# Kernel tuning notes

Hardware: AMD Instinct MI355X
Metric: run time of the kernel (lower is better)

Reference implementation:

```python
import jax, jax.numpy as jnp
import numpy as np

BRANCH = 4
DEPTH = 8  # complete 4-ary tree, levels 0..8 (leaves are level 0)
X_SIZE = 512
H_SIZE = 512


def _build_tree():
    N = sum(BRANCH ** d for d in range(DEPTH + 1))  # 87381
    depth = np.zeros(N, dtype=np.int32)
    start = 1
    for d in range(1, DEPTH + 1):
        c = BRANCH ** d
        depth[start:start + c] = d
        start += c
    node_level = (DEPTH - depth).astype(np.int32)  # topological height, leaves=0
    src = np.arange(1, N, dtype=np.int32)          # child
    dst = (src - 1) // BRANCH                      # parent
    return N, src, dst.astype(np.int32), node_level


def setup_inputs() -> dict:
    key = jax.random.key(0)
    k = jax.random.split(key, 6)
    N, src, dst, node_level = _build_tree()
    sx = 1.0 / np.sqrt(X_SIZE)
    sh = 1.0 / np.sqrt(H_SIZE)
    return {
        "x": jax.random.normal(k[0], (N, X_SIZE), jnp.float32),
        "W_w": jax.random.normal(k[1], (3 * H_SIZE, X_SIZE), jnp.float32) * sx,
        "b_w": jax.random.normal(k[2], (3 * H_SIZE,), jnp.float32) * sx,
        "U_r": jax.random.normal(k[3], (H_SIZE, H_SIZE), jnp.float32) * sh,
        "U_hc": jax.random.normal(k[4], (H_SIZE, H_SIZE), jnp.float32) * sh,
        "U_z": jax.random.normal(k[5], (H_SIZE, H_SIZE), jnp.float32) * sh,
        "edge_src": jnp.asarray(src),
        "edge_dst": jnp.asarray(dst),
        "node_level": jnp.asarray(node_level),
        "num_levels": DEPTH + 1,
    }


def reference(x, W_w, b_w, U_r, U_hc, U_z, edge_src, edge_dst, node_level, num_levels):
    hs = U_r.shape[0]
    n = x.shape[0]
    wx = x @ W_w.T + b_w                      # (n, 3h)
    wrx = wx[:, :hs]
    whx = wx[:, hs:2 * hs]
    wzx = wx[:, 2 * hs:]
    edge_level = node_level[edge_dst]         # level of parent receiving the message

    # Leaves: mailbox is a single zero 'z' slot -> z = sigmoid(w_z_x), h_pre = 0
    h_leaf = (1.0 - jax.nn.sigmoid(wzx)) * jnp.tanh(whx)
    h = jnp.where((node_level == 0)[:, None], h_leaf, 0.0)

    for l in range(1, num_levels):
        emask = (edge_level == l).astype(x.dtype)[:, None]   # (E,1)
        hsrc = h[edge_src] * emask                            # masked child states (E,h)
        h_sum = jax.ops.segment_sum(hsrc, edge_dst, num_segments=n)  # sum of children
        r = jax.nn.sigmoid(wrx + h_sum @ U_r.T)
        h_cand = jnp.tanh(whx + (r * h_sum) @ U_hc.T)
        z_e = hsrc @ U_z.T                                    # raw U_z(h_child), (E,h)
        # reduce: h_pre = sum_children z_raw * h_child (no sigmoid, faithful to source)
        h_pre = jax.ops.segment_sum(z_e * hsrc, edge_dst, num_segments=n)
        # update: z = sigmoid(z_raw + w_z_x), summed over children
        z_sig_sum = jax.ops.segment_sum(
            jax.nn.sigmoid(z_e + wzx[edge_dst]) * emask, edge_dst, num_segments=n)
        h_new = h_pre + (1.0 - z_sig_sum) * h_cand
        h = jnp.where((node_level == l)[:, None], h_new, h)
    return h
```

## Files before the change

### kernel.cpp

```cpp
#include <hip/hip_runtime.h>


#define NNODES 87381
#define NINT   21845
#define NLEAF  65536

typedef __attribute__((ext_vector_type(8))) __bf16 bf16x8;
typedef __attribute__((ext_vector_type(4))) float f32x4;

__device__ __forceinline__ float sigmoidf_(float x) { return 1.0f / (1.0f + __expf(-x)); }
__device__ __forceinline__ float tanhf_(float x) { return 2.0f / (1.0f + __expf(-2.0f * x)) - 1.0f; }

__device__ __forceinline__ unsigned short bf_rne(float f) {
  unsigned int u = __float_as_uint(f);
  unsigned int r = u + 0x7FFFu + ((u >> 16) & 1u);
  return (unsigned short)(r >> 16);
}
__device__ __forceinline__ void split2(float f, unsigned short& h, unsigned short& l) {
  h = bf_rne(f);
  l = bf_rne(f - __uint_as_float((unsigned int)h << 16));
}
__device__ __forceinline__ float bf2f(unsigned short h) {
  return __uint_as_float((unsigned int)h << 16);
}

__device__ __forceinline__ int xcd_remap(int h, int nwg) {
  const int q = nwg >> 3, r = nwg & 7;
  const int xcd = h & 7, slot = h >> 3;
  return (xcd < r ? xcd * (q + 1) : r * (q + 1) + (xcd - r) * q) + slot;
}

__global__ __launch_bounds__(256) void split_k(const float* __restrict__ s,
                                               unsigned short* __restrict__ hi,
                                               unsigned short* __restrict__ lo, int n4) {
  int i = blockIdx.x * 256 + threadIdx.x;
  if (i >= n4) return;
  float4 v = *(const float4*)(s + (size_t)i * 4);
  ushort4 h, l;
  split2(v.x, h.x, l.x); split2(v.y, h.y, l.y);
  split2(v.z, h.z, l.z); split2(v.w, h.w, l.w);
  *(ushort4*)(hi + (size_t)i * 4) = h;
  *(ushort4*)(lo + (size_t)i * 4) = l;
}

template <bool CLAMP>
__device__ __forceinline__ void stage_half(const unsigned short* __restrict__ g,
                                           int rows_left, unsigned short* l0,
                                           int lane, int c0) {
#pragma unroll
  for (int c = c0; c < c0 + 4; ++c) {
    const int lr = c * 16 + (lane >> 2);
    const int gr = CLAMP ? (lr < rows_left ? lr : rows_left - 1) : lr;
    const int sg = (lane & 3) ^ ((lr >> 1) & 3);
    __builtin_amdgcn_global_load_lds(
        (const __attribute__((address_space(1))) void*)(g + (size_t)gr * 512 + sg * 8),
        (__attribute__((address_space(3))) void*)(l0 + c * 512), 16, 0, 0);
  }
}

template <int EPI>
__global__ __launch_bounds__(512, 4) void mgemm(const unsigned short* __restrict__ Ah,
                                                const unsigned short* __restrict__ Al,
                                                const unsigned short* __restrict__ Bh,
                                                const unsigned short* __restrict__ Bl,
                                                float* __restrict__ C, int ldc, int M,
                                                const float* __restrict__ wx, int g0,
                                                const float* __restrict__ bias,
                                                const unsigned short* __restrict__ FH,
                                                const unsigned short* __restrict__ FL,
                                                unsigned short* __restrict__ Oh,
                                                unsigned short* __restrict__ Ol,
                                                int nnb) {
  __shared__ unsigned short As_h[2][128][32];
  __shared__ unsigned short As_l[2][128][32];
  __shared__ unsigned short Bs_h[2][128][32];
  __shared__ unsigned short Bs_l[2][128][32];
  const int t = threadIdx.x;
  const int lane = t & 63, wave = t >> 6;
  const int wm = wave & 1, wn = wave >> 1;
  const int L = xcd_remap(blockIdx.x, gridDim.x);
  const int m0 = (L / nnb) * 128, n0 = (L % nnb) * 128;

  f32x4 acc[4][2];
#pragma unroll
  for (int i = 0; i < 4; ++i)
#pragma unroll
    for (int j = 0; j < 2; ++j) acc[i][j] = (f32x4){0.f, 0.f, 0.f, 0.f};

  const int fr = lane & 15, fg = lane >> 4;

  auto stage = [&](int buf, int k0) {
    const int c0 = (wave & 1) * 4;
    switch (wave >> 1) {
      case 0: stage_half<true >(Ah + (size_t)m0 * 512 + k0, M - m0, &As_h[buf][0][0], lane, c0); break;
      case 1: stage_half<true >(Al + (size_t)m0 * 512 + k0, M - m0, &As_l[buf][0][0], lane, c0); break;
      case 2: stage_half<false>(Bh + (size_t)n0 * 512 + k0, 0, &Bs_h[buf][0][0], lane, c0); break;
      default: stage_half<false>(Bl + (size_t)n0 * 512 + k0, 0, &Bs_l[buf][0][0], lane, c0); break;
    }
  };

  auto comp = [&](int buf) {
    bf16x8 ah[4], al[4], bh[2], bl[2];
#pragma unroll
    for (int mt = 0; mt < 4; ++mt) {
      const int row = wm * 64 + mt * 16 + fr;
      const int gp = (fg ^ ((row >> 1) & 3)) * 8;
      ah[mt] = *(const bf16x8*)&As_h[buf][row][gp];
      al[mt] = *(const bf16x8*)&As_l[buf][row][gp];
    }
#pragma unroll
    for (int nt = 0; nt < 2; ++nt) {
      const int row = wn * 32 + nt * 16 + fr;
      const int gp = (fg ^ ((row >> 1) & 3)) * 8;
      bh[nt] = *(const bf16x8*)&Bs_h[buf][row][gp];
      bl[nt] = *(const bf16x8*)&Bs_l[buf][row][gp];
    }
#pragma unroll
    for (int mt = 0; mt < 4; ++mt)
#pragma unroll
      for (int nt = 0; nt < 2; ++nt) {
        acc[mt][nt] = __builtin_amdgcn_mfma_f32_16x16x32_bf16(ah[mt], bh[nt], acc[mt][nt], 0, 0, 0);
        acc[mt][nt] = __builtin_amdgcn_mfma_f32_16x16x32_bf16(ah[mt], bl[nt], acc[mt][nt], 0, 0, 0);
        acc[mt][nt] = __builtin_amdgcn_mfma_f32_16x16x32_bf16(al[mt], bh[nt], acc[mt][nt], 0, 0, 0);
      }
  };

  stage(0, 0);
  __syncthreads();
  for (int kk = 0; kk < 16; kk += 2) {
    stage(1, (kk + 1) * 32);
    comp(0);
    __syncthreads();
    if (kk < 14) stage(0, (kk + 2) * 32);
    comp(1);
    __syncthreads();
  }

  const int ecol = lane & 15;
  const int erow = (lane >> 4) * 4;

  if (EPI == 4) {
#pragma unroll
    for (int mt = 0; mt < 4; ++mt) {
#pragma unroll
      for (int nt = 0; nt < 2; ++nt) {
        const int col = n0 + wn * 32 + nt * 16 + ecol;
        const int row0 = m0 + wm * 64 + mt * 16 + erow;
        if (row0 >= M) continue;
        const int p = row0 >> 2;
        const float wz = wx[(size_t)(g0 + p) * 1536 + 1024 + col];
        float hpre = 0.f, zs = 0.f;
#pragma unroll
        for (int r = 0; r < 4; ++r) {
          const float zev = acc[mt][nt][r];
          const float hch = bias[(size_t)(row0 + r) * 512 + col];
          hpre = fmaf(zev, hch, hpre);
          zs += sigmoidf_(zev + wz);
        }
        float* po = C + (size_t)p * 512 + col;
        const float hc = *po;
        const float res = hpre + (1.f - zs) * hc;
        *po = res;
        unsigned short oh, ol;
        split2(res, oh, ol);
        Oh[(size_t)p * 512 + col] = oh;
        Ol[(size_t)p * 512 + col] = ol;
      }
    }
    return;
  }

#pragma unroll
  for (int mt = 0; mt < 4; ++mt) {
#pragma unroll
    for (int nt = 0; nt < 2; ++nt) {
      const int col = n0 + wn * 32 + nt * 16 + ecol;
#pragma unroll
      for (int r = 0; r < 4; ++r) {
        const int row = m0 + wm * 64 + mt * 16 + erow + r;
        if (row >= M) continue;
        const float v = acc[mt][nt][r];
        if (EPI == 1) {
          const size_t ix = (size_t)row * 512 + col;
          const float hs = bf2f(FH[ix]) + bf2f(FL[ix]);
          const float rg = sigmoidf_(wx[(size_t)(g0 + row) * 1536 + col] + v);
          unsigned short oh, ol;
          split2(rg * hs, oh, ol);
          Oh[ix] = oh;
          Ol[ix] = ol;
        } else if (EPI == 2) {
          C[(size_t)row * ldc + col] = tanhf_(wx[(size_t)(g0 + row) * 1536 + 512 + col] + v);
        } else {
          C[(size_t)row * ldc + col] = v + bias[col];
        }
      }
    }
  }
}

__global__ __launch_bounds__(512, 4) void mleaf(const unsigned short* __restrict__ xh,
                                                const unsigned short* __restrict__ xl,
                                                const unsigned short* __restrict__ Wh,
                                                const unsigned short* __restrict__ Wl,
                                                const float* __restrict__ bw,
                                                float* __restrict__ out,
                                                unsigned short* __restrict__ hcH,
                                                unsigned short* __restrict__ hcL) {
  __shared__ unsigned short As_h[2][128][32];
  __shared__ unsigned short As_l[2][128][32];
  __shared__ unsigned short Bs_h[2][128][32];
  __shared__ unsigned short Bs_l[2][128][32];
  const int t = threadIdx.x;
  const int lane = t & 63, wave = t >> 6;
  const int wm = wave & 1, wn = wave >> 1;
  const int L = xcd_remap(blockIdx.x, gridDim.x);
  const int m0 = (L >> 3) * 128, n0 = (L & 7) * 64;

  f32x4 acch[4], accz[4];
#pragma unroll
  for (int i = 0; i < 4; ++i) {
    acch[i] = (f32x4){0.f, 0.f, 0.f, 0.f};
    accz[i] = (f32x4){0.f, 0.f, 0.f, 0.f};
  }

  const int fr = lane & 15, fg = lane >> 4;

  auto stage = [&](int buf, int k0) {
    const int c0 = (wave & 1) * 4;
    const int grp = wave >> 1;
    if (grp == 0) {
      stage_half<false>(xh + (size_t)m0 * 512 + k0, 0, &As_h[buf][0][0], lane, c0);
    } else if (grp == 1) {
      stage_half<false>(xl + (size_t)m0 * 512 + k0, 0, &As_l[buf][0][0], lane, c0);
    } else {
      const unsigned short* Ws = (grp == 2) ? Wh : Wl;
      unsigned short* dst = (grp == 2) ? &Bs_h[buf][0][0] : &Bs_l[buf][0][0];
#pragma unroll
      for (int c = c0; c < c0 + 4; ++c) {
        const int lr = c * 16 + (lane >> 2);
        const int grow = (lr < 64) ? (512 + n0 + lr) : (1024 + n0 + (lr - 64));
        const int sg = (lane & 3) ^ ((lr >> 1) & 3);
        __builtin_amdgcn_global_load_lds(
            (const __attribute__((address_space(1))) void*)(Ws + (size_t)grow * 512 + k0 + sg * 8),
            (__attribute__((address_space(3))) void*)(dst + c * 512), 16, 0, 0);
      }
    }
  };

  auto comp = [&](int buf) {
    bf16x8 ah[4], al[4], bhh, bhl, bzh, bzl;
    {
      const int rh_ = wn * 16 + fr;
      const int rz_ = 64 + rh_;
      const int gph = (fg ^ ((rh_ >> 1) & 3)) * 8;
      const int gpz = (fg ^ ((rz_ >> 1) & 3)) * 8;
      bhh = *(const bf16x8*)&Bs_h[buf][rh_][gph];
      bhl = *(const bf16x8*)&Bs_l[buf][rh_][gph];
      bzh = *(const bf16x8*)&Bs_h[buf][rz_][gpz];
      bzl = *(const bf16x8*)&Bs_l[buf][rz_][gpz];
    }
#pragma unroll
    for (int mt = 0; mt < 4; ++mt) {
      const int row = wm * 64 + mt * 16 + fr;
      const int gp = (fg ^ ((row >> 1) & 3)) * 8;
      ah[mt] = *(const bf16x8*)&As_h[buf][row][gp];
      al[mt] = *(const bf16x8*)&As_l[buf][row][gp];
    }
#pragma unroll
    for (int mt = 0; mt < 4; ++mt) {
      acch[mt] = __builtin_amdgcn_mfma_f32_16x16x32_bf16(ah[mt], bhh, acch[mt], 0, 0, 0);
      acch[mt] = __builtin_amdgcn_mfma_f32_16x16x32_bf16(ah[mt], bhl, acch[mt], 0, 0, 0);
      acch[mt] = __builtin_amdgcn_mfma_f32_16x16x32_bf16(al[mt], bhh, acch[mt], 0, 0, 0);
      accz[mt] = __builtin_amdgcn_mfma_f32_16x16x32_bf16(ah[mt], bzh, accz[mt], 0, 0, 0);
      accz[mt] = __builtin_amdgcn_mfma_f32_16x16x32_bf16(ah[mt], bzl, accz[mt], 0, 0, 0);
      accz[mt] = __builtin_amdgcn_mfma_f32_16x16x32_bf16(al[mt], bzh, accz[mt], 0, 0, 0);
    }
  };

  stage(0, 0);
  __syncthreads();
  for (int kk = 0; kk < 16; kk += 2) {
    stage(1, (kk + 1) * 32);
    comp(0);
    __syncthreads();
    if (kk < 14) stage(0, (kk + 2) * 32);
    comp(1);
    __syncthreads();
  }

  const int ecol = lane & 15;
  const int erow = (lane >> 4) * 4;
  const int col = n0 + wn * 16 + ecol;
  const float bh_ = bw[512 + col];
  const float bz_ = bw[1024 + col];
#pragma unroll
  for (int mt = 0; mt < 4; ++mt) {
#pragma unroll
    for (int r = 0; r < 4; ++r) {
      const int row = m0 + wm * 64 + mt * 16 + erow + r;
      const float vh = acch[mt][r] + bh_;
      const float vz = accz[mt][r] + bz_;
      const float hval = (1.f - sigmoidf_(vz)) * tanhf_(vh);
      out[(size_t)(NINT + row) * 512 + col] = hval;
      unsigned short oh, ol;
      split2(hval, oh, ol);
      const size_t ix = (size_t)row * 512 + col;
      hcH[ix] = oh;
      hcL[ix] = ol;
    }
  }
}

__global__ __launch_bounds__(256) void child_sum_k(const float* __restrict__ out,
                                                   int cbase, int nl,
                                                   unsigned short* __restrict__ hH,
                                                   unsigned short* __restrict__ hL) {
  const int idx = blockIdx.x * 256 + threadIdx.x;
  if (idx >= nl * 128) return;
  const int i = idx >> 7;
  const int jq = (idx & 127) << 2;
  const float* b = out + (size_t)(cbase + 4 * i) * 512 + jq;
  const float4 a = *(const float4*)(b);
  const float4 c = *(const float4*)(b + 512);
  const float4 d = *(const float4*)(b + 1024);
  const float4 e = *(const float4*)(b + 1536);
  float4 s;
  s.x = a.x + c.x + d.x + e.x;
  s.y = a.y + c.y + d.y + e.y;
  s.z = a.z + c.z + d.z + e.z;
  s.w = a.w + c.w + d.w + e.w;
  ushort4 sh, sl;
  split2(s.x, sh.x, sl.x); split2(s.y, sh.y, sl.y);
  split2(s.z, sh.z, sl.z); split2(s.w, sh.w, sl.w);
  *(ushort4*)(hH + (size_t)i * 512 + jq) = sh;
  *(ushort4*)(hL + (size_t)i * 512 + jq) = sl;
}

extern "C" void kernel_launch(void* const* d_in, const int* in_sizes, int n_in,
                              void* d_out, int out_size, void* d_ws, size_t ws_size,
                              hipStream_t stream) {
  const float* x   = (const float*)d_in[0];
  const float* Ww  = (const float*)d_in[1];
  const float* bw  = (const float*)d_in[2];
  const float* Ur  = (const float*)d_in[3];
  const float* Uhc = (const float*)d_in[4];
  const float* Uz  = (const float*)d_in[5];
  float* out = (float*)d_out;

  char* p = (char*)d_ws;
  unsigned short* x_hi = (unsigned short*)p;
  unsigned short* x_lo = x_hi + (size_t)NNODES * 512;
  unsigned short* rhH = (unsigned short*)p;
  unsigned short* rhL = rhH + (size_t)16384 * 512;
  p += (size_t)NNODES * 512 * 4;
  float* wx_int = (float*)p;                 p += (size_t)NINT * 1536 * 4;
  unsigned short* hsH = (unsigned short*)p;  p += (size_t)16384 * 512 * 2;
  unsigned short* hsL = (unsigned short*)p;  p += (size_t)16384 * 512 * 2;
  unsigned short* hcH = (unsigned short*)p;  p += (size_t)65536 * 512 * 2;
  unsigned short* hcL = (unsigned short*)p;  p += (size_t)65536 * 512 * 2;
  unsigned short* hc2H = (unsigned short*)p; p += (size_t)16384 * 512 * 2;
  unsigned short* hc2L = (unsigned short*)p; p += (size_t)16384 * 512 * 2;
  unsigned short* W_hi = (unsigned short*)p;   p += (size_t)1536 * 512 * 2;
  unsigned short* W_lo = (unsigned short*)p;   p += (size_t)1536 * 512 * 2;
  unsigned short* Ur_hi = (unsigned short*)p;  p += (size_t)512 * 512 * 2;
  unsigned short* Ur_lo = (unsigned short*)p;  p += (size_t)512 * 512 * 2;
  unsigned short* Uhc_hi = (unsigned short*)p; p += (size_t)512 * 512 * 2;
  unsigned short* Uhc_lo = (unsigned short*)p; p += (size_t)512 * 512 * 2;
  unsigned short* Uz_hi = (unsigned short*)p;  p += (size_t)512 * 512 * 2;
  unsigned short* Uz_lo = (unsigned short*)p;  p += (size_t)512 * 512 * 2;

  split_k<<<(1536 * 512 / 4 + 255) / 256, 256, 0, stream>>>(Ww, W_hi, W_lo, 1536 * 512 / 4);
  split_k<<<(512 * 512 / 4 + 255) / 256, 256, 0, stream>>>(Ur, Ur_hi, Ur_lo, 512 * 512 / 4);
  split_k<<<(512 * 512 / 4 + 255) / 256, 256, 0, stream>>>(Uhc, Uhc_hi, Uhc_lo, 512 * 512 / 4);
  split_k<<<(512 * 512 / 4 + 255) / 256, 256, 0, stream>>>(Uz, Uz_hi, Uz_lo, 512 * 512 / 4);
  split_k<<<((int)((size_t)NNODES * 512 / 4) + 255) / 256, 256, 0, stream>>>(
      x, x_hi, x_lo, (int)((size_t)NNODES * 512 / 4));

  mgemm<3><<<((NINT + 127) / 128) * 12, 512, 0, stream>>>(
      x_hi, x_lo, W_hi, W_lo, wx_int, 1536, NINT, nullptr, 0, bw,
      nullptr, nullptr, nullptr, nullptr, 12);

  mleaf<<<(NLEAF / 128) * 8, 512, 0, stream>>>(
      x_hi + (size_t)NINT * 512, x_lo + (size_t)NINT * 512, W_hi, W_lo, bw, out, hcH, hcL);

  static const int S[10] = {0, 1, 5, 21, 85, 341, 1365, 5461, 21845, 87381};
  unsigned short *rdH = hcH, *rdL = hcL, *wrH = hc2H, *wrL = hc2L;
  for (int l = 1; l <= 8; ++l) {
    const int d = 8 - l;
    const int pbase = S[d];
    const int nl = S[d + 1] - S[d];
    const int cbase = S[d + 1];
    const int el = 4 * nl;

    child_sum_k<<<(nl * 128 + 255) / 256, 256, 0, stream>>>(out, cbase, nl, hsH, hsL);

    const int grm = (nl + 127) / 128;
    mgemm<1><<<grm * 4, 512, 0, stream>>>(hsH, hsL, Ur_hi, Ur_lo, nullptr, 512, nl,
                                          wx_int, pbase, nullptr, hsH, hsL, rhH, rhL, 4);
    mgemm<2><<<grm * 4, 512, 0, stream>>>(rhH, rhL, Uhc_hi, Uhc_lo,
                                          out + (size_t)pbase * 512, 512, nl,
                                          wx_int, pbase, nullptr, nullptr, nullptr,
                                          nullptr, nullptr, 4);
    const int gzm = (el + 127) / 128;
    mgemm<4><<<gzm * 4, 512, 0, stream>>>(rdH, rdL, Uz_hi, Uz_lo,
                                          out + (size_t)pbase * 512, 512, el,
                                          wx_int, pbase, out + (size_t)cbase * 512,
                                          nullptr, nullptr, wrH, wrL, 4);
    unsigned short* tH = rdH; rdH = wrH; wrH = tH;
    unsigned short* tL = rdL; rdL = wrL; wrL = tL;
  }
}
```

Before: 1.420 ms.

## Fuse the last four small tree levels into one single-block persistent kernel

Levels 5 through 8 of the tree have only 64, 16, 4 and 1 parent nodes. These were previously handled by 16 separate kernel launches, each mostly idle. A single 1024-thread block now runs the child sum, the three GEMMs and their epilogues for these levels, with block-wide barriers between stages. This removes launch and tail latency, at the cost of running the small GEMMs on one compute unit, where each wave must stream the full weight matrices from memory.

```diff
diff --git a/kernel.cpp b/kernel.cpp
--- a/kernel.cpp
+++ b/kernel.cpp
@@ -336,6 +336,153 @@
   *(ushort4*)(hL + (size_t)i * 512 + jq) = sl;
 }
 
+__device__ __forceinline__ void tail_gemm(
+    int M, const unsigned short* __restrict__ AH, const unsigned short* __restrict__ AL,
+    const unsigned short* __restrict__ BH, const unsigned short* __restrict__ BL,
+    int wave, int lane, int epi, const float* __restrict__ wx, int g0,
+    float* __restrict__ C, const unsigned short* __restrict__ FH,
+    const unsigned short* __restrict__ FL, unsigned short* __restrict__ OH,
+    unsigned short* __restrict__ OL, const float* __restrict__ childh) {
+  const int fr = lane & 15, fq = (lane >> 4) * 8;
+  const int n0 = wave * 32;
+  const int ecol = lane & 15, erow = (lane >> 4) * 4;
+  for (int mc = 0; mc < M; mc += 64) {
+    f32x4 acc[4][2];
+#pragma unroll
+    for (int i = 0; i < 4; ++i) {
+      acc[i][0] = (f32x4){0.f, 0.f, 0.f, 0.f};
+      acc[i][1] = (f32x4){0.f, 0.f, 0.f, 0.f};
+    }
+#pragma unroll 2
+    for (int k0 = 0; k0 < 512; k0 += 32) {
+      bf16x8 ah[4], al[4], bh[2], bl[2];
+#pragma unroll
+      for (int nt = 0; nt < 2; ++nt) {
+        const size_t bo = (size_t)(n0 + nt * 16 + fr) * 512 + k0 + fq;
+        bh[nt] = *(const bf16x8*)(BH + bo);
+        bl[nt] = *(const bf16x8*)(BL + bo);
+      }
+#pragma unroll
+      for (int mt = 0; mt < 4; ++mt) {
+        int row = mc + mt * 16 + fr;
+        if (row >= M) row = M - 1;
+        const size_t ao = (size_t)row * 512 + k0 + fq;
+        ah[mt] = *(const bf16x8*)(AH + ao);
+        al[mt] = *(const bf16x8*)(AL + ao);
+      }
+#pragma unroll
+      for (int mt = 0; mt < 4; ++mt)
+#pragma unroll
+        for (int nt = 0; nt < 2; ++nt) {
+          acc[mt][nt] = __builtin_amdgcn_mfma_f32_16x16x32_bf16(ah[mt], bh[nt], acc[mt][nt], 0, 0, 0);
+          acc[mt][nt] = __builtin_amdgcn_mfma_f32_16x16x32_bf16(ah[mt], bl[nt], acc[mt][nt], 0, 0, 0);
+          acc[mt][nt] = __builtin_amdgcn_mfma_f32_16x16x32_bf16(al[mt], bh[nt], acc[mt][nt], 0, 0, 0);
+        }
+    }
+#pragma unroll
+    for (int mt = 0; mt < 4; ++mt) {
+#pragma unroll
+      for (int nt = 0; nt < 2; ++nt) {
+        const int col = n0 + nt * 16 + ecol;
+        if (epi == 4) {
+          const int row0 = mc + mt * 16 + erow;
+          if (row0 >= M) continue;
+          const int p = row0 >> 2;
+          const float wz = wx[(size_t)(g0 + p) * 1536 + 1024 + col];
+          float hpre = 0.f, zs = 0.f;
+#pragma unroll
+          for (int r = 0; r < 4; ++r) {
+            const float zev = acc[mt][nt][r];
+            hpre = fmaf(zev, childh[(size_t)(row0 + r) * 512 + col], hpre);
+            zs += sigmoidf_(zev + wz);
+          }
+          float* po = C + (size_t)p * 512 + col;
+          const float res = hpre + (1.f - zs) * (*po);
+          *po = res;
+          unsigned short oh, ol;
+          split2(res, oh, ol);
+          OH[(size_t)p * 512 + col] = oh;
+          OL[(size_t)p * 512 + col] = ol;
+        } else {
+#pragma unroll
+          for (int r = 0; r < 4; ++r) {
+            const int row = mc + mt * 16 + erow + r;
+            if (row >= M) continue;
+            const float v = acc[mt][nt][r];
+            if (epi == 1) {
+              const size_t ix = (size_t)row * 512 + col;
+              const float hs = bf2f(FH[ix]) + bf2f(FL[ix]);
+              const float rg = sigmoidf_(wx[(size_t)(g0 + row) * 1536 + col] + v);
+              unsigned short oh, ol;
+              split2(rg * hs, oh, ol);
+              OH[ix] = oh;
+              OL[ix] = ol;
+            } else {
+              C[(size_t)row * 512 + col] = tanhf_(wx[(size_t)(g0 + row) * 1536 + 512 + col] + v);
+            }
+          }
+        }
+      }
+    }
+  }
+}
+
+__global__ __launch_bounds__(1024) void tail_k(
+    float* __restrict__ out, const float* __restrict__ wx,
+    const unsigned short* __restrict__ UrH, const unsigned short* __restrict__ UrL,
+    const unsigned short* __restrict__ UhH, const unsigned short* __restrict__ UhL,
+    const unsigned short* __restrict__ UzH, const unsigned short* __restrict__ UzL,
+    unsigned short* __restrict__ hsH, unsigned short* __restrict__ hsL,
+    unsigned short* __restrict__ rhH, unsigned short* __restrict__ rhL,
+    unsigned short* __restrict__ aH, unsigned short* __restrict__ aL,
+    unsigned short* __restrict__ bH, unsigned short* __restrict__ bL) {
+  const int t = threadIdx.x;
+  const int lane = t & 63, wave = t >> 6;
+  const int PB[4] = {21, 5, 1, 0};
+  const int NL[4] = {64, 16, 4, 1};
+  const int CB[4] = {85, 21, 5, 1};
+  unsigned short *rdH = aH, *rdL = aL, *wrH = bH, *wrL = bL;
+  for (int li = 0; li < 4; ++li) {
+    const int pbase = PB[li], nl = NL[li], cbase = CB[li];
+    for (int idx = t; idx < nl * 128; idx += 1024) {
+      const int i = idx >> 7;
+      const int jq = (idx & 127) << 2;
+      const float* b = out + (size_t)(cbase + 4 * i) * 512 + jq;
+      const float4 a = *(const float4*)(b);
+      const float4 c = *(const float4*)(b + 512);
+      const float4 d = *(const float4*)(b + 1024);
+      const float4 e = *(const float4*)(b + 1536);
+      float4 s;
+      s.x = a.x + c.x + d.x + e.x;
+      s.y = a.y + c.y + d.y + e.y;
+      s.z = a.z + c.z + d.z + e.z;
+      s.w = a.w + c.w + d.w + e.w;
+      ushort4 sh, sl;
+      split2(s.x, sh.x, sl.x); split2(s.y, sh.y, sl.y);
+      split2(s.z, sh.z, sl.z); split2(s.w, sh.w, sl.w);
+      *(ushort4*)(hsH + (size_t)i * 512 + jq) = sh;
+      *(ushort4*)(hsL + (size_t)i * 512 + jq) = sl;
+    }
+    __threadfence();
+    __syncthreads();
+    tail_gemm(nl, hsH, hsL, UrH, UrL, wave, lane, 1, wx, pbase,
+              nullptr, hsH, hsL, rhH, rhL, nullptr);
+    __threadfence();
+    __syncthreads();
+    tail_gemm(nl, rhH, rhL, UhH, UhL, wave, lane, 2, wx, pbase,
+              out + (size_t)pbase * 512, nullptr, nullptr, nullptr, nullptr, nullptr);
+    __threadfence();
+    __syncthreads();
+    tail_gemm(nl * 4, rdH, rdL, UzH, UzL, wave, lane, 4, wx, pbase,
+              out + (size_t)pbase * 512, nullptr, nullptr, wrH, wrL,
+              out + (size_t)cbase * 512);
+    __threadfence();
+    __syncthreads();
+    unsigned short* tH = rdH; rdH = wrH; wrH = tH;
+    unsigned short* tL = rdL; rdL = wrL; wrL = tL;
+  }
+}
+
 extern "C" void kernel_launch(void* const* d_in, const int* in_sizes, int n_in,
                               void* d_out, int out_size, void* d_ws, size_t ws_size,
                               hipStream_t stream) {
@@ -371,8 +518,8 @@
 
   split_k<<<(1536 * 512 / 4 + 255) / 256, 256, 0, stream>>>(Ww, W_hi, W_lo, 1536 * 512 / 4);
   split_k<<<(512 * 512 / 4 + 255) / 256, 256, 0, stream>>>(Ur, Ur_hi, Ur_lo, 512 * 512 / 4);
+  split_k<<<(512 * 512 / 4 + 255) / 256, 256, 0, stream>>>(Uz, Uz_hi, Uz_lo, 512 * 512 / 4);
   split_k<<<(512 * 512 / 4 + 255) / 256, 256, 0, stream>>>(Uhc, Uhc_hi, Uhc_lo, 512 * 512 / 4);
-  split_k<<<(512 * 512 / 4 + 255) / 256, 256, 0, stream>>>(Uz, Uz_hi, Uz_lo, 512 * 512 / 4);
   split_k<<<((int)((size_t)NNODES * 512 / 4) + 255) / 256, 256, 0, stream>>>(
       x, x_hi, x_lo, (int)((size_t)NNODES * 512 / 4));
 
@@ -385,7 +532,7 @@
 
   static const int S[10] = {0, 1, 5, 21, 85, 341, 1365, 5461, 21845, 87381};
   unsigned short *rdH = hcH, *rdL = hcL, *wrH = hc2H, *wrL = hc2L;
-  for (int l = 1; l <= 8; ++l) {
+  for (int l = 1; l <= 4; ++l) {
     const int d = 8 - l;
     const int pbase = S[d];
     const int nl = S[d + 1] - S[d];
@@ -409,4 +556,8 @@
     unsigned short* tH = rdH; rdH = wrH; wrH = tH;
     unsigned short* tL = rdL; rdL = wrL; wrL = tL;
   }
-}
+
+  tail_k<<<1, 1024, 0, stream>>>(out, wx_int, Ur_hi, Ur_lo, Uhc_hi, Uhc_lo,
+                                 Uz_hi, Uz_lo, hsH, hsL, rhH, rhL,
+                                 rdH, rdL, wrH, wrL);
+}
```

After: 2.625 ms. 1.85x slower.
